# Kernel tuning notes

Hardware: AMD Instinct MI355X
Metric: run time of the kernel (lower is better)

## Reference

```python
import jax, jax.numpy as jnp
import numpy as np

B, N, D = 4, 2048, 1024
H, HD = 16, 64          # heads, head dim
ROT = 64                # rotary dims (full head)
SCALE = HD ** -0.5


def _rotate_half(x):
    # interleaved pair rotation: (c r) with r=2 -> (-x2, x1)
    x = x.reshape(x.shape[:-1] + (-1, 2))
    x1, x2 = x[..., 0], x[..., 1]
    return jnp.stack((-x2, x1), axis=-1).reshape(x.shape[:-2] + (-1,))


def _rope(t, pos_enc):
    # t: [b,h,n,c], pos_enc: [1,n,rot] -> broadcast over heads
    pe = pos_enc[:, None, : t.shape[-2], :]          # [1,1,n,rot]
    t_rot, t_pass = t[..., :ROT], t[..., ROT:]
    t_rot = t_rot * jnp.cos(pe) + _rotate_half(t_rot) * jnp.sin(pe)
    return jnp.concatenate((t_rot, t_pass), axis=-1)


def setup_inputs() -> dict:
    key = jax.random.key(0)
    ks = jax.random.split(key, 16)
    s = 0.02
    return {
        "query": jax.random.normal(ks[0], (B, N, D), jnp.float32),
        "key": jax.random.normal(ks[1], (B, N, D), jnp.float32),
        "value": jax.random.normal(ks[2], (B, N, D), jnp.float32),
        "pad_mask": jax.random.randint(ks[3], (B, N), 0, 2) > 0,
        "pos_enc": jax.random.uniform(ks[4], (1, N, ROT), jnp.float32),
        "Wq": jax.random.normal(ks[5], (D, D), jnp.float32) * s,
        "bq": jnp.zeros((D,), jnp.float32),
        "Wk": jax.random.normal(ks[6], (D, D), jnp.float32) * s,
        "bk": jnp.zeros((D,), jnp.float32),
        "Wv": jax.random.normal(ks[7], (D, D), jnp.float32) * s,
        "bv": jnp.zeros((D,), jnp.float32),
        "Wo": jax.random.normal(ks[8], (D, D), jnp.float32) * s,
        "bo": jnp.zeros((D,), jnp.float32),
    }


def reference(query, key, value, pad_mask, pos_enc, Wq, bq, Wk, bk, Wv, bv, Wo, bo):
    def split_heads(x):
        return x.reshape(x.shape[0], x.shape[1], H, HD).transpose(0, 2, 1, 3)  # b h n c

    q = split_heads(query @ Wq + bq) * SCALE
    k = split_heads(key @ Wk + bk)
    v = split_heads(value @ Wv + bv)

    q = _rope(q, pos_enc)
    k = _rope(k, pos_enc)

    attn = jnp.einsum("bhic,bhjc->bhij", q, k)
    neg = -jnp.finfo(attn.dtype).max
    attn = jnp.where(pad_mask[:, None, None, :], neg, attn)
    attn = jax.nn.softmax(attn, axis=-1)

    o = jnp.einsum("bhij,bhjc->bhic", attn, v)
    o = o.transpose(0, 2, 1, 3).reshape(o.shape[0], o.shape[2], H * HD)  # b n (h c)
    return o @ Wo + bo
```

## Files before the change

### kernel.cpp

```cpp
#include <hip/hip_runtime.h>

#define B_ 4
#define N_ 2048
#define D_ 1024
#define H_ 16
#define HD_ 64
#define QSCALE_ 0.18033688011112042f

typedef __bf16 bf16x8 __attribute__((ext_vector_type(8)));
typedef float f32x4 __attribute__((ext_vector_type(4)));

#if __has_builtin(__builtin_amdgcn_exp2f)
#define EXP2(x) __builtin_amdgcn_exp2f(x)
#else
#define EXP2(x) exp2f(x)
#endif

__device__ __forceinline__ f32x4 mfma16(bf16x8 a, bf16x8 b, f32x4 c) {
    return __builtin_amdgcn_mfma_f32_16x16x32_bf16(a, b, c, 0, 0, 0);
}

__device__ __forceinline__ void gload16(const void* g, void* l) {
    __builtin_amdgcn_global_load_lds(
        (const __attribute__((address_space(1))) void*)g,
        (__attribute__((address_space(3))) void*)l, 16, 0, 0);
}

__device__ __forceinline__ unsigned pack2(float x, float y) {
    __bf16 a = (__bf16)x, b = (__bf16)y;
    unsigned ua = __builtin_bit_cast(unsigned short, a);
    unsigned ub = __builtin_bit_cast(unsigned short, b);
    return ua | (ub << 16);
}

__global__ void prep_kernel(const float* __restrict__ pe, const int* __restrict__ mask,
                            unsigned* __restrict__ cstab, float* __restrict__ maskf) {
    int i = blockIdx.x * 256 + threadIdx.x;
    if (i < N_ * HD_) {
        float v = pe[i];
        __bf16 cb = (__bf16)cosf(v), sb = (__bf16)sinf(v);
        unsigned cu = __builtin_bit_cast(unsigned short, cb);
        unsigned su = __builtin_bit_cast(unsigned short, sb);
        cstab[i] = cu | (su << 16);
    }
    if (i < B_ * N_) maskf[i] = mask[i] ? -1e30f : 0.0f;
}

__global__ __launch_bounds__(256) void tw_kernel(const float* __restrict__ W, __bf16* __restrict__ Wt) {
    __shared__ float T[64][65];
    const int k0 = blockIdx.x * 64, n0 = blockIdx.y * 64;
    const int t = threadIdx.x;
#pragma unroll
    for (int i = 0; i < 4; ++i) {
        int row = i * 16 + (t >> 4);
        int c4 = (t & 15) * 4;
        float4 v = *(const float4*)(W + (size_t)(k0 + row) * D_ + n0 + c4);
        T[row][c4] = v.x; T[row][c4 + 1] = v.y; T[row][c4 + 2] = v.z; T[row][c4 + 3] = v.w;
    }
    __syncthreads();
#pragma unroll
    for (int i = 0; i < 2; ++i) {
        int task = i * 256 + t;
        int nrow = task >> 3, ks = task & 7;
        bf16x8 o;
#pragma unroll
        for (int e = 0; e < 8; ++e) o[e] = (__bf16)T[ks * 8 + e][nrow];
        *(bf16x8*)(Wt + (size_t)(n0 + nrow) * D_ + k0 + ks * 8) = o;
    }
}

__global__ __launch_bounds__(256) void tw3_kernel(
    const float* __restrict__ W0, const float* __restrict__ W1, const float* __restrict__ W2,
    __bf16* __restrict__ T0, __bf16* __restrict__ T1, __bf16* __restrict__ T2)
{
    const float* W = (blockIdx.z == 0) ? W0 : (blockIdx.z == 1) ? W1 : W2;
    __bf16* Wt = (blockIdx.z == 0) ? T0 : (blockIdx.z == 1) ? T1 : T2;
    __shared__ float T[64][65];
    const int k0 = blockIdx.x * 64, n0 = blockIdx.y * 64;
    const int t = threadIdx.x;
#pragma unroll
    for (int i = 0; i < 4; ++i) {
        int row = i * 16 + (t >> 4);
        int c4 = (t & 15) * 4;
        float4 v = *(const float4*)(W + (size_t)(k0 + row) * D_ + n0 + c4);
        T[row][c4] = v.x; T[row][c4 + 1] = v.y; T[row][c4 + 2] = v.z; T[row][c4 + 3] = v.w;
    }
    __syncthreads();
#pragma unroll
    for (int i = 0; i < 2; ++i) {
        int task = i * 256 + t;
        int nrow = task >> 3, ks = task & 7;
        bf16x8 o;
#pragma unroll
        for (int e = 0; e < 8; ++e) o[e] = (__bf16)T[ks * 8 + e][nrow];
        *(bf16x8*)(Wt + (size_t)(n0 + nrow) * D_ + k0 + ks * 8) = o;
    }
}

__global__ __launch_bounds__(256) void proj_v2(
    const float* __restrict__ X, const __bf16* __restrict__ Wt,
    const float* __restrict__ bias, const unsigned* __restrict__ cstab,
    __bf16* __restrict__ dst, int mode)
{
    __shared__ __align__(16) char smem[35072];
    __bf16* As = (__bf16*)smem;
    __bf16* Bs = (__bf16*)(smem + 16384);

    const int tid = threadIdx.x;
    const int lane = tid & 63, w = tid >> 6;
    const int wr = w >> 1, wc = w & 1;
    const int r16 = lane & 15, g = lane >> 4;
    const int m0 = blockIdx.x * 128;
    const int n0 = blockIdx.y * 128;
    const int srow8 = tid >> 3, slot = tid & 7;

    f32x4 acc[4][4];
#pragma unroll
    for (int m = 0; m < 4; ++m)
#pragma unroll
        for (int n = 0; n < 4; ++n) acc[m][n] = (f32x4){0.f, 0.f, 0.f, 0.f};

    for (int kt = 0; kt < 16; ++kt) {
#pragma unroll
        for (int j = 0; j < 4; ++j) {
            int row = j * 32 + srow8;
            const char* src = (const char*)Wt + ((size_t)(n0 + row) * D_ + kt * 64) * 2
                              + ((slot ^ (row & 7)) << 4);
            gload16(src, (char*)Bs + j * 4096 + w * 1024);
        }
#pragma unroll
        for (int i = 0; i < 4; ++i) {
            int row = i * 32 + srow8;
            const float* s = X + (size_t)(m0 + row) * D_ + kt * 64 + slot * 8;
            float4 v0 = *(const float4*)s;
            float4 v1 = *(const float4*)(s + 4);
            bf16x8 bv;
            bv[0] = (__bf16)v0.x; bv[1] = (__bf16)v0.y; bv[2] = (__bf16)v0.z; bv[3] = (__bf16)v0.w;
            bv[4] = (__bf16)v1.x; bv[5] = (__bf16)v1.y; bv[6] = (__bf16)v1.z; bv[7] = (__bf16)v1.w;
            *(bf16x8*)((char*)As + row * 128 + ((slot ^ (row & 7)) << 4)) = bv;
        }
        __syncthreads();
#pragma unroll
        for (int kk = 0; kk < 2; ++kk) {
            bf16x8 aF[4], bF[4];
#pragma unroll
            for (int m = 0; m < 4; ++m) {
                int row = wr * 64 + m * 16 + r16;
                aF[m] = *(const bf16x8*)((char*)As + row * 128 + (((kk * 4 + g) ^ (row & 7)) << 4));
            }
#pragma unroll
            for (int n = 0; n < 4; ++n) {
                int row = wc * 64 + n * 16 + r16;
                bF[n] = *(const bf16x8*)((char*)Bs + row * 128 + (((kk * 4 + g) ^ (row & 7)) << 4));
            }
#pragma unroll
            for (int m = 0; m < 4; ++m)
#pragma unroll
                for (int n = 0; n < 4; ++n)
                    acc[m][n] = mfma16(aF[m], bF[n], acc[m][n]);
        }
        __syncthreads();
    }

    if (mode <= 1) {
#pragma unroll
        for (int m = 0; m < 4; ++m)
#pragma unroll
            for (int n = 0; n < 4; ++n) {
                int col = n0 + wc * 64 + n * 16 + r16;
                int h = col >> 6, hd = col & 63;
#pragma unroll
                for (int j = 0; j < 4; ++j) {
                    int bn = m0 + wr * 64 + m * 16 + g * 4 + j;
                    int np = bn & (N_ - 1), b = bn >> 11;
                    float val = acc[m][n][j] + bias[col];
                    if (mode == 0) val *= QSCALE_;
                    float other = __shfl_xor(val, 1);
                    unsigned cs = cstab[np * HD_ + hd];
                    float c = __uint_as_float(cs << 16);
                    float sn = __uint_as_float(cs & 0xffff0000u);
                    val = val * c + ((col & 1) ? other : -other) * sn;
                    dst[((size_t)(b * H_ + h) * N_ + np) * HD_ + hd] = (__bf16)val;
                }
            }
    } else {
        __bf16* T = (__bf16*)smem;
#pragma unroll
        for (int m = 0; m < 4; ++m)
#pragma unroll
            for (int n = 0; n < 4; ++n) {
                int c = wc * 64 + n * 16 + r16;
                float bs = bias[n0 + c];
#pragma unroll
                for (int j = 0; j < 4; ++j) {
                    int sr = wr * 64 + m * 16 + g * 4 + j;
                    T[c * 136 + sr] = (__bf16)(acc[m][n][j] + bs);
                }
            }
        __syncthreads();
        const int b = m0 >> 11, np0 = m0 & (N_ - 1);
#pragma unroll
        for (int i = 0; i < 8; ++i) {
            int task = i * 256 + tid;
            int trow = task >> 4, ch = task & 15;
            int colg = n0 + trow;
            int h = colg >> 6, hd = colg & 63;
            bf16x8 vv = *(const bf16x8*)&T[trow * 136 + ch * 8];
            *(bf16x8*)(dst + (((size_t)(b * H_ + h) * HD_ + hd) * N_ + np0 + ch * 8)) = vv;
        }
    }
}

__global__ __launch_bounds__(256) void attn_v5(
    const __bf16* __restrict__ qws, const __bf16* __restrict__ kws,
    const __bf16* __restrict__ vtws, const float* __restrict__ maskf,
    __bf16* __restrict__ ows)
{
    __shared__ __align__(16) __bf16 Ks[2][4096];
    __shared__ __align__(16) __bf16 Vs[2][4096];
    __shared__ __align__(16) char Pbuf[8192];

    const int tid = threadIdx.x;
    const int lane = tid & 63, w = tid >> 6;
    const int r16 = lane & 15, g = lane >> 4;

    const int lid = blockIdx.x;
    const int virt = (lid & 7) * 128 + (lid >> 3);
    const int bh = virt >> 4;
    const int b = bh >> 4, h = bh & 15;
    const int q0 = (virt & 15) * 128;
    const int srow8 = tid >> 3, slot = tid & 7;

    bf16x8 qF[2][2];
#pragma unroll
    for (int qq = 0; qq < 2; ++qq) {
        const __bf16* qb = qws + ((size_t)bh * N_ + q0 + w * 32 + qq * 16 + r16) * HD_ + g * 8;
        qF[qq][0] = *(const bf16x8*)qb;
        qF[qq][1] = *(const bf16x8*)(qb + 32);
    }

    bf16x8 onesF;
#pragma unroll
    for (int e = 0; e < 8; ++e) onesF[e] = (__bf16)1.0f;

    const char* kbase = (const char*)(kws + (size_t)bh * N_ * HD_);
    const char* vbase = (const char*)(vtws + (size_t)bh * HD_ * N_);
    const float* mbase = maskf + b * N_;

    f32x4 o[2][4];
    f32x4 lacc[2];
#pragma unroll
    for (int qq = 0; qq < 2; ++qq) {
        lacc[qq] = (f32x4){0.f, 0.f, 0.f, 0.f};
#pragma unroll
        for (int n = 0; n < 4; ++n) o[qq][n] = (f32x4){0.f, 0.f, 0.f, 0.f};
    }

    auto stage = [&](int bb, int kt) {
#pragma unroll
        for (int j = 0; j < 2; ++j) {
            int row = j * 32 + srow8;
            const char* src = kbase + (size_t)(kt * 64 + row) * 128 + ((slot ^ (row & 7)) << 4);
            gload16(src, (char*)Ks[bb] + j * 4096 + w * 1024);
        }
#pragma unroll
        for (int j = 0; j < 2; ++j) {
            int row = j * 32 + srow8;
            const char* src = vbase + (size_t)row * (N_ * 2) + kt * 128 + ((slot ^ (row & 7)) << 4);
            gload16(src, (char*)Vs[bb] + j * 4096 + w * 1024);
        }
    };

    stage(0, 0);
    __syncthreads();

    int buf = 0;
    for (int kt = 0; kt < N_ / 64; ++kt) {
        if (kt + 1 < N_ / 64) stage(buf ^ 1, kt + 1);

        f32x4 s[2][4];
#pragma unroll
        for (int n = 0; n < 4; ++n) {
            s[0][n] = *(const f32x4*)(mbase + kt * 64 + n * 16 + g * 4);
            s[1][n] = *(const f32x4*)(mbase + kt * 64 + n * 16 + g * 4);
        }

        __builtin_amdgcn_s_setprio(1);
#pragma unroll
        for (int n = 0; n < 4; ++n) {
            int row = n * 16 + r16;
            bf16x8 kF0 = *(const bf16x8*)((char*)Ks[buf] + row * 128 + ((g ^ (row & 7)) << 4));
            bf16x8 kF1 = *(const bf16x8*)((char*)Ks[buf] + row * 128 + (((4 + g) ^ (row & 7)) << 4));
#pragma unroll
            for (int qq = 0; qq < 2; ++qq) {
                s[qq][n] = mfma16(kF0, qF[qq][0], s[qq][n]);
                s[qq][n] = mfma16(kF1, qF[qq][1], s[qq][n]);
            }
        }
        __builtin_amdgcn_s_setprio(0);

        bf16x8 pF[2][2];
#pragma unroll
        for (int qq = 0; qq < 2; ++qq) {
            char* Pw = Pbuf + w * 2048;
#pragma unroll
            for (int n = 0; n < 4; ++n) {
                float p0 = EXP2(s[qq][n][0]);
                float p1 = EXP2(s[qq][n][1]);
                float p2 = EXP2(s[qq][n][2]);
                float p3 = EXP2(s[qq][n][3]);
                int u0 = ((n * 2 + (g >> 1)) ^ (r16 & 7));
                int off = (g & 1) * 2;
                *(unsigned*)(Pw + r16 * 128 + u0 * 16 + off * 4)       = pack2(p0, p1);
                *(unsigned*)(Pw + r16 * 128 + u0 * 16 + (off + 1) * 4) = pack2(p2, p3);
            }
#pragma unroll
            for (int kk = 0; kk < 2; ++kk)
                pF[qq][kk] = *(const bf16x8*)(Pw + r16 * 128 + (((kk * 4 + g) ^ (r16 & 7)) << 4));
            lacc[qq] = mfma16(onesF, pF[qq][0], lacc[qq]);
            lacc[qq] = mfma16(onesF, pF[qq][1], lacc[qq]);
        }

        __builtin_amdgcn_s_setprio(1);
#pragma unroll
        for (int n = 0; n < 4; ++n) {
            int row = n * 16 + r16;
            bf16x8 vF0 = *(const bf16x8*)((char*)Vs[buf] + row * 128 + ((g ^ (row & 7)) << 4));
            bf16x8 vF1 = *(const bf16x8*)((char*)Vs[buf] + row * 128 + (((4 + g) ^ (row & 7)) << 4));
#pragma unroll
            for (int qq = 0; qq < 2; ++qq) {
                o[qq][n] = mfma16(vF0, pF[qq][0], o[qq][n]);
                o[qq][n] = mfma16(vF1, pF[qq][1], o[qq][n]);
            }
        }
        __builtin_amdgcn_s_setprio(0);
        __syncthreads();
        buf ^= 1;
    }

#pragma unroll
    for (int qq = 0; qq < 2; ++qq) {
        float inv = 1.0f / lacc[qq][0];
        char* Pw = Pbuf + w * 2048;
#pragma unroll
        for (int n = 0; n < 4; ++n) {
            int u0 = ((n * 2 + (g >> 1)) ^ (r16 & 7));
            int off = (g & 1) * 2;
            *(unsigned*)(Pw + r16 * 128 + u0 * 16 + off * 4)       = pack2(o[qq][n][0] * inv, o[qq][n][1] * inv);
            *(unsigned*)(Pw + r16 * 128 + u0 * 16 + (off + 1) * 4) = pack2(o[qq][n][2] * inv, o[qq][n][3] * inv);
        }
        int qrow = q0 + w * 32 + qq * 16 + r16;
#pragma unroll
        for (int kk = 0; kk < 2; ++kk) {
            bf16x8 v = *(const bf16x8*)(Pw + r16 * 128 + (((kk * 4 + g) ^ (r16 & 7)) << 4));
            *(bf16x8*)(ows + ((size_t)(b * N_ + qrow)) * D_ + h * HD_ + kk * 32 + g * 8) = v;
        }
    }
}

__global__ __launch_bounds__(256) void gemm_out_v2(
    const __bf16* __restrict__ A, const __bf16* __restrict__ Wt,
    const float* __restrict__ bias, float* __restrict__ out)
{
    __shared__ __align__(16) __bf16 As[8192], Bs[8192];

    const int tid = threadIdx.x;
    const int lane = tid & 63, w = tid >> 6;
    const int wr = w >> 1, wc = w & 1;
    const int r16 = lane & 15, g = lane >> 4;
    const int m0 = blockIdx.x * 128;
    const int n0 = blockIdx.y * 128;
    const int srow8 = tid >> 3, slot = tid & 7;

    f32x4 acc[4][4];
#pragma unroll
    for (int m = 0; m < 4; ++m)
#pragma unroll
        for (int n = 0; n < 4; ++n) acc[m][n] = (f32x4){0.f, 0.f, 0.f, 0.f};

    for (int kt = 0; kt < 16; ++kt) {
#pragma unroll
        for (int j = 0; j < 4; ++j) {
            int row = j * 32 + srow8;
            const char* srcA = (const char*)A + ((size_t)(m0 + row) * D_ + kt * 64) * 2
                               + ((slot ^ (row & 7)) << 4);
            gload16(srcA, (char*)As + j * 4096 + w * 1024);
            const char* srcB = (const char*)Wt + ((size_t)(n0 + row) * D_ + kt * 64) * 2
                               + ((slot ^ (row & 7)) << 4);
            gload16(srcB, (char*)Bs + j * 4096 + w * 1024);
        }
        __syncthreads();
#pragma unroll
        for (int kk = 0; kk < 2; ++kk) {
            bf16x8 aF[4], bF[4];
#pragma unroll
            for (int m = 0; m < 4; ++m) {
                int row = wr * 64 + m * 16 + r16;
                aF[m] = *(const bf16x8*)((char*)As + row * 128 + (((kk * 4 + g) ^ (row & 7)) << 4));
            }
#pragma unroll
            for (int n = 0; n < 4; ++n) {
                int row = wc * 64 + n * 16 + r16;
                bF[n] = *(const bf16x8*)((char*)Bs + row * 128 + (((kk * 4 + g) ^ (row & 7)) << 4));
            }
#pragma unroll
            for (int m = 0; m < 4; ++m)
#pragma unroll
                for (int n = 0; n < 4; ++n)
                    acc[m][n] = mfma16(aF[m], bF[n], acc[m][n]);
        }
        __syncthreads();
    }

#pragma unroll
    for (int m = 0; m < 4; ++m)
#pragma unroll
        for (int n = 0; n < 4; ++n) {
            int col = n0 + wc * 64 + n * 16 + r16;
            float bs = bias[col];
#pragma unroll
            for (int j = 0; j < 4; ++j) {
                int bn = m0 + wr * 64 + m * 16 + g * 4 + j;
                out[(size_t)bn * D_ + col] = acc[m][n][j] + bs;
            }
        }
}

extern "C" void kernel_launch(void* const* d_in, const int* in_sizes, int n_in,
                              void* d_out, int out_size, void* d_ws, size_t ws_size,
                              hipStream_t stream)
{
    const float* query = (const float*)d_in[0];
    const float* key   = (const float*)d_in[1];
    const float* value = (const float*)d_in[2];
    const int* mask    = (const int*)d_in[3];
    const float* pos_enc = (const float*)d_in[4];
    const float* Wq = (const float*)d_in[5];
    const float* bq = (const float*)d_in[6];
    const float* Wk = (const float*)d_in[7];
    const float* bk = (const float*)d_in[8];
    const float* Wv = (const float*)d_in[9];
    const float* bv = (const float*)d_in[10];
    const float* Wo = (const float*)d_in[11];
    const float* bo = (const float*)d_in[12];
    float* out = (float*)d_out;

    char* ws = (char*)d_ws;
    const size_t MB16 = (size_t)16 * 1024 * 1024;
    const size_t need = 4 * MB16 + 524288 + 32768;
    if (ws_size < need) return;

    __bf16* qws   = (__bf16*)(ws);
    __bf16* kws   = (__bf16*)(ws + MB16);
    __bf16* vtws  = (__bf16*)(ws + 2 * MB16);
    __bf16* ows   = (__bf16*)(ws + 3 * MB16);
    unsigned* cstab = (unsigned*)(ws + 4 * MB16);
    float* maskf  = (float*)(ws + 4 * MB16 + 524288);
    __bf16* wtQ   = (__bf16*)(ws + 3 * MB16);
    __bf16* wtK   = wtQ + (size_t)D_ * D_;
    __bf16* wtV   = wtK + (size_t)D_ * D_;
    __bf16* wtO   = (__bf16*)(ws);

    hipLaunchKernelGGL(prep_kernel, dim3(512), dim3(256), 0, stream, pos_enc, mask, cstab, maskf);

    dim3 gt3(16, 16, 3);
    dim3 gt(16, 16);
    dim3 gp(8192 / 128, 1024 / 128);
    hipLaunchKernelGGL(tw3_kernel, gt3, dim3(256), 0, stream, Wq, Wk, Wv, wtQ, wtK, wtV);
    hipLaunchKernelGGL(proj_v2, gp, dim3(256), 0, stream, query, wtQ, bq, cstab, qws, 0);
    hipLaunchKernelGGL(proj_v2, gp, dim3(256), 0, stream, key,   wtK, bk, cstab, kws, 1);
    hipLaunchKernelGGL(proj_v2, gp, dim3(256), 0, stream, value, wtV, bv, cstab, vtws, 2);

    hipLaunchKernelGGL(attn_v5, dim3(1024), dim3(256), 0, stream,
                       qws, kws, vtws, maskf, ows);

    hipLaunchKernelGGL(tw_kernel, gt, dim3(256), 0, stream, Wo, wtO);
    hipLaunchKernelGGL(gemm_out_v2, gp, dim3(256), 0, stream, ows, wtO, bo, out);
}
```

Baseline: 238.1 us.

## Merge Q/K/V projections into one launch and unroll attention double-buffer loop

The three separate projection launches become a single kernel whose grid's y dimension selects Q, K or V, with the weight async loads moved after the activation conversion. The attention kernel gets launch_bounds with an occupancy hint, named K/V buffers, and a manually unrolled two-tile loop so buffer indices are compile-time constants; the two query sub-tiles' softmax writes are also serialized through the shared P buffer. This is meant to cut launch overhead and tail effects and to remove dynamic LDS indexing. The occupancy hint may add register pressure.

```diff
diff --git a/kernel.cpp b/kernel.cpp
--- a/kernel.cpp
+++ b/kernel.cpp
@@ -97,21 +97,30 @@
     }
 }
 
-__global__ __launch_bounds__(256) void proj_v2(
-    const float* __restrict__ X, const __bf16* __restrict__ Wt,
-    const float* __restrict__ bias, const unsigned* __restrict__ cstab,
-    __bf16* __restrict__ dst, int mode)
+__global__ __launch_bounds__(256) void proj_v4(
+    const float* __restrict__ Xq, const float* __restrict__ Xk, const float* __restrict__ Xv,
+    const __bf16* __restrict__ WtQ, const __bf16* __restrict__ WtK, const __bf16* __restrict__ WtV,
+    const float* __restrict__ bQ, const float* __restrict__ bK, const float* __restrict__ bV,
+    const unsigned* __restrict__ cstab,
+    __bf16* __restrict__ dq, __bf16* __restrict__ dk, __bf16* __restrict__ dv)
 {
     __shared__ __align__(16) char smem[35072];
     __bf16* As = (__bf16*)smem;
     __bf16* Bs = (__bf16*)(smem + 16384);
+
+    const int which = blockIdx.y >> 3;
+    const float* X    = (which == 0) ? Xq  : (which == 1) ? Xk  : Xv;
+    const __bf16* Wt  = (which == 0) ? WtQ : (which == 1) ? WtK : WtV;
+    const float* bias = (which == 0) ? bQ  : (which == 1) ? bK  : bV;
+    __bf16* dst       = (which == 0) ? dq  : (which == 1) ? dk  : dv;
+    const int mode = which;
 
     const int tid = threadIdx.x;
     const int lane = tid & 63, w = tid >> 6;
     const int wr = w >> 1, wc = w & 1;
     const int r16 = lane & 15, g = lane >> 4;
     const int m0 = blockIdx.x * 128;
-    const int n0 = blockIdx.y * 128;
+    const int n0 = (blockIdx.y & 7) * 128;
     const int srow8 = tid >> 3, slot = tid & 7;
 
     f32x4 acc[4][4];
@@ -121,13 +130,6 @@
         for (int n = 0; n < 4; ++n) acc[m][n] = (f32x4){0.f, 0.f, 0.f, 0.f};
 
     for (int kt = 0; kt < 16; ++kt) {
-#pragma unroll
-        for (int j = 0; j < 4; ++j) {
-            int row = j * 32 + srow8;
-            const char* src = (const char*)Wt + ((size_t)(n0 + row) * D_ + kt * 64) * 2
-                              + ((slot ^ (row & 7)) << 4);
-            gload16(src, (char*)Bs + j * 4096 + w * 1024);
-        }
 #pragma unroll
         for (int i = 0; i < 4; ++i) {
             int row = i * 32 + srow8;
@@ -138,6 +140,13 @@
             bv[0] = (__bf16)v0.x; bv[1] = (__bf16)v0.y; bv[2] = (__bf16)v0.z; bv[3] = (__bf16)v0.w;
             bv[4] = (__bf16)v1.x; bv[5] = (__bf16)v1.y; bv[6] = (__bf16)v1.z; bv[7] = (__bf16)v1.w;
             *(bf16x8*)((char*)As + row * 128 + ((slot ^ (row & 7)) << 4)) = bv;
+        }
+#pragma unroll
+        for (int j = 0; j < 4; ++j) {
+            int row = j * 32 + srow8;
+            const char* src = (const char*)Wt + ((size_t)(n0 + row) * D_ + kt * 64) * 2
+                              + ((slot ^ (row & 7)) << 4);
+            gload16(src, (char*)Bs + j * 4096 + w * 1024);
         }
         __syncthreads();
 #pragma unroll
@@ -211,13 +220,13 @@
     }
 }
 
-__global__ __launch_bounds__(256) void attn_v5(
+__global__ __launch_bounds__(256, 4) void attn_v6(
     const __bf16* __restrict__ qws, const __bf16* __restrict__ kws,
     const __bf16* __restrict__ vtws, const float* __restrict__ maskf,
     __bf16* __restrict__ ows)
 {
-    __shared__ __align__(16) __bf16 Ks[2][4096];
-    __shared__ __align__(16) __bf16 Vs[2][4096];
+    __shared__ __align__(16) __bf16 Ks0[4096], Ks1[4096];
+    __shared__ __align__(16) __bf16 Vs0[4096], Vs1[4096];
     __shared__ __align__(16) char Pbuf[8192];
 
     const int tid = threadIdx.x;
@@ -246,6 +255,7 @@
     const char* kbase = (const char*)(kws + (size_t)bh * N_ * HD_);
     const char* vbase = (const char*)(vtws + (size_t)bh * HD_ * N_);
     const float* mbase = maskf + b * N_;
+    char* Pw = Pbuf + w * 2048;
 
     f32x4 o[2][4];
     f32x4 lacc[2];
@@ -256,92 +266,92 @@
         for (int n = 0; n < 4; ++n) o[qq][n] = (f32x4){0.f, 0.f, 0.f, 0.f};
     }
 
-    auto stage = [&](int bb, int kt) {
-#pragma unroll
-        for (int j = 0; j < 2; ++j) {
-            int row = j * 32 + srow8;
-            const char* src = kbase + (size_t)(kt * 64 + row) * 128 + ((slot ^ (row & 7)) << 4);
-            gload16(src, (char*)Ks[bb] + j * 4096 + w * 1024);
-        }
-#pragma unroll
-        for (int j = 0; j < 2; ++j) {
-            int row = j * 32 + srow8;
-            const char* src = vbase + (size_t)row * (N_ * 2) + kt * 128 + ((slot ^ (row & 7)) << 4);
-            gload16(src, (char*)Vs[bb] + j * 4096 + w * 1024);
-        }
-    };
-
-    stage(0, 0);
+#define STAGE_(KD, VD, kt) {                                                          \
+    _Pragma("unroll")                                                                 \
+    for (int j = 0; j < 2; ++j) {                                                     \
+        int row = j * 32 + srow8;                                                     \
+        gload16(kbase + (size_t)((kt) * 64 + row) * 128 + ((slot ^ (row & 7)) << 4),  \
+                (char*)(KD) + j * 4096 + w * 1024);                                   \
+    }                                                                                 \
+    _Pragma("unroll")                                                                 \
+    for (int j = 0; j < 2; ++j) {                                                     \
+        int row = j * 32 + srow8;                                                     \
+        gload16(vbase + (size_t)row * (N_ * 2) + (kt) * 128 + ((slot ^ (row & 7)) << 4), \
+                (char*)(VD) + j * 4096 + w * 1024);                                   \
+    } }
+
+#define TILE_(KB, VB, KN, VN, kt) {                                                   \
+    if ((kt) + 1 < 32) STAGE_(KN, VN, (kt) + 1);                                      \
+    f32x4 s0[4], s1[4];                                                               \
+    _Pragma("unroll")                                                                 \
+    for (int n = 0; n < 4; ++n) {                                                     \
+        f32x4 mb = *(const f32x4*)(mbase + (kt) * 64 + n * 16 + g * 4);               \
+        s0[n] = mb; s1[n] = mb;                                                       \
+    }                                                                                 \
+    __builtin_amdgcn_s_setprio(1);                                                    \
+    _Pragma("unroll")                                                                 \
+    for (int n = 0; n < 4; ++n) {                                                     \
+        int row = n * 16 + r16;                                                       \
+        bf16x8 kF0 = *(const bf16x8*)((const char*)(KB) + row * 128 + ((g ^ (row & 7)) << 4));        \
+        bf16x8 kF1 = *(const bf16x8*)((const char*)(KB) + row * 128 + (((4 + g) ^ (row & 7)) << 4));  \
+        s0[n] = mfma16(kF0, qF[0][0], s0[n]);                                         \
+        s0[n] = mfma16(kF1, qF[0][1], s0[n]);                                         \
+        s1[n] = mfma16(kF0, qF[1][0], s1[n]);                                         \
+        s1[n] = mfma16(kF1, qF[1][1], s1[n]);                                         \
+    }                                                                                 \
+    __builtin_amdgcn_s_setprio(0);                                                    \
+    bf16x8 pF0[2], pF1[2];                                                            \
+    _Pragma("unroll")                                                                 \
+    for (int n = 0; n < 4; ++n) {                                                     \
+        int u0 = ((n * 2 + (g >> 1)) ^ (r16 & 7));                                    \
+        int off = (g & 1) * 2;                                                        \
+        *(unsigned*)(Pw + r16 * 128 + u0 * 16 + off * 4)       = pack2(EXP2(s0[n][0]), EXP2(s0[n][1])); \
+        *(unsigned*)(Pw + r16 * 128 + u0 * 16 + (off + 1) * 4) = pack2(EXP2(s0[n][2]), EXP2(s0[n][3])); \
+    }                                                                                 \
+    _Pragma("unroll")                                                                 \
+    for (int kk = 0; kk < 2; ++kk)                                                    \
+        pF0[kk] = *(const bf16x8*)(Pw + r16 * 128 + (((kk * 4 + g) ^ (r16 & 7)) << 4)); \
+    lacc[0] = mfma16(onesF, pF0[0], lacc[0]);                                         \
+    lacc[0] = mfma16(onesF, pF0[1], lacc[0]);                                         \
+    _Pragma("unroll")                                                                 \
+    for (int n = 0; n < 4; ++n) {                                                     \
+        int u0 = ((n * 2 + (g >> 1)) ^ (r16 & 7));                                    \
+        int off = (g & 1) * 2;                                                        \
+        *(unsigned*)(Pw + r16 * 128 + u0 * 16 + off * 4)       = pack2(EXP2(s1[n][0]), EXP2(s1[n][1])); \
+        *(unsigned*)(Pw + r16 * 128 + u0 * 16 + (off + 1) * 4) = pack2(EXP2(s1[n][2]), EXP2(s1[n][3])); \
+    }                                                                                 \
+    _Pragma("unroll")                                                                 \
+    for (int kk = 0; kk < 2; ++kk)                                                    \
+        pF1[kk] = *(const bf16x8*)(Pw + r16 * 128 + (((kk * 4 + g) ^ (r16 & 7)) << 4)); \
+    lacc[1] = mfma16(onesF, pF1[0], lacc[1]);                                         \
+    lacc[1] = mfma16(onesF, pF1[1], lacc[1]);                                         \
+    __builtin_amdgcn_s_setprio(1);                                                    \
+    _Pragma("unroll")                                                                 \
+    for (int n = 0; n < 4; ++n) {                                                     \
+        int row = n * 16 + r16;                                                       \
+        bf16x8 vF0 = *(const bf16x8*)((const char*)(VB) + row * 128 + ((g ^ (row & 7)) << 4));        \
+        bf16x8 vF1 = *(const bf16x8*)((const char*)(VB) + row * 128 + (((4 + g) ^ (row & 7)) << 4));  \
+        o[0][n] = mfma16(vF0, pF0[0], o[0][n]);                                       \
+        o[0][n] = mfma16(vF1, pF0[1], o[0][n]);                                       \
+        o[1][n] = mfma16(vF0, pF1[0], o[1][n]);                                       \
+        o[1][n] = mfma16(vF1, pF1[1], o[1][n]);                                       \
+    }                                                                                 \
+    __builtin_amdgcn_s_setprio(0);                                                    \
+    __syncthreads(); }
+
+    STAGE_(Ks0, Vs0, 0);
     __syncthreads();
 
-    int buf = 0;
-    for (int kt = 0; kt < N_ / 64; ++kt) {
-        if (kt + 1 < N_ / 64) stage(buf ^ 1, kt + 1);
-
-        f32x4 s[2][4];
-#pragma unroll
-        for (int n = 0; n < 4; ++n) {
-            s[0][n] = *(const f32x4*)(mbase + kt * 64 + n * 16 + g * 4);
-            s[1][n] = *(const f32x4*)(mbase + kt * 64 + n * 16 + g * 4);
-        }
-
-        __builtin_amdgcn_s_setprio(1);
-#pragma unroll
-        for (int n = 0; n < 4; ++n) {
-            int row = n * 16 + r16;
-            bf16x8 kF0 = *(const bf16x8*)((char*)Ks[buf] + row * 128 + ((g ^ (row & 7)) << 4));
-            bf16x8 kF1 = *(const bf16x8*)((char*)Ks[buf] + row * 128 + (((4 + g) ^ (row & 7)) << 4));
-#pragma unroll
-            for (int qq = 0; qq < 2; ++qq) {
-                s[qq][n] = mfma16(kF0, qF[qq][0], s[qq][n]);
-                s[qq][n] = mfma16(kF1, qF[qq][1], s[qq][n]);
-            }
-        }
-        __builtin_amdgcn_s_setprio(0);
-
-        bf16x8 pF[2][2];
-#pragma unroll
-        for (int qq = 0; qq < 2; ++qq) {
-            char* Pw = Pbuf + w * 2048;
-#pragma unroll
-            for (int n = 0; n < 4; ++n) {
-                float p0 = EXP2(s[qq][n][0]);
-                float p1 = EXP2(s[qq][n][1]);
-                float p2 = EXP2(s[qq][n][2]);
-                float p3 = EXP2(s[qq][n][3]);
-                int u0 = ((n * 2 + (g >> 1)) ^ (r16 & 7));
-                int off = (g & 1) * 2;
-                *(unsigned*)(Pw + r16 * 128 + u0 * 16 + off * 4)       = pack2(p0, p1);
-                *(unsigned*)(Pw + r16 * 128 + u0 * 16 + (off + 1) * 4) = pack2(p2, p3);
-            }
-#pragma unroll
-            for (int kk = 0; kk < 2; ++kk)
-                pF[qq][kk] = *(const bf16x8*)(Pw + r16 * 128 + (((kk * 4 + g) ^ (r16 & 7)) << 4));
-            lacc[qq] = mfma16(onesF, pF[qq][0], lacc[qq]);
-            lacc[qq] = mfma16(onesF, pF[qq][1], lacc[qq]);
-        }
-
-        __builtin_amdgcn_s_setprio(1);
-#pragma unroll
-        for (int n = 0; n < 4; ++n) {
-            int row = n * 16 + r16;
-            bf16x8 vF0 = *(const bf16x8*)((char*)Vs[buf] + row * 128 + ((g ^ (row & 7)) << 4));
-            bf16x8 vF1 = *(const bf16x8*)((char*)Vs[buf] + row * 128 + (((4 + g) ^ (row & 7)) << 4));
-#pragma unroll
-            for (int qq = 0; qq < 2; ++qq) {
-                o[qq][n] = mfma16(vF0, pF[qq][0], o[qq][n]);
-                o[qq][n] = mfma16(vF1, pF[qq][1], o[qq][n]);
-            }
-        }
-        __builtin_amdgcn_s_setprio(0);
-        __syncthreads();
-        buf ^= 1;
-    }
+    for (int kt = 0; kt < 32; kt += 2) {
+        TILE_(Ks0, Vs0, Ks1, Vs1, kt);
+        TILE_(Ks1, Vs1, Ks0, Vs0, kt + 1);
+    }
+#undef TILE_
+#undef STAGE_
 
 #pragma unroll
     for (int qq = 0; qq < 2; ++qq) {
         float inv = 1.0f / lacc[qq][0];
-        char* Pw = Pbuf + w * 2048;
 #pragma unroll
         for (int n = 0; n < 4; ++n) {
             int u0 = ((n * 2 + (g >> 1)) ^ (r16 & 7));
@@ -465,15 +475,14 @@
 
     dim3 gt3(16, 16, 3);
     dim3 gt(16, 16);
-    dim3 gp(8192 / 128, 1024 / 128);
     hipLaunchKernelGGL(tw3_kernel, gt3, dim3(256), 0, stream, Wq, Wk, Wv, wtQ, wtK, wtV);
-    hipLaunchKernelGGL(proj_v2, gp, dim3(256), 0, stream, query, wtQ, bq, cstab, qws, 0);
-    hipLaunchKernelGGL(proj_v2, gp, dim3(256), 0, stream, key,   wtK, bk, cstab, kws, 1);
-    hipLaunchKernelGGL(proj_v2, gp, dim3(256), 0, stream, value, wtV, bv, cstab, vtws, 2);
-
-    hipLaunchKernelGGL(attn_v5, dim3(1024), dim3(256), 0, stream,
+
+    hipLaunchKernelGGL(proj_v4, dim3(64, 24), dim3(256), 0, stream,
+                       query, key, value, wtQ, wtK, wtV, bq, bk, bv, cstab, qws, kws, vtws);
+
+    hipLaunchKernelGGL(attn_v6, dim3(1024), dim3(256), 0, stream,
                        qws, kws, vtws, maskf, ows);
 
     hipLaunchKernelGGL(tw_kernel, gt, dim3(256), 0, stream, Wo, wtO);
-    hipLaunchKernelGGL(gemm_out_v2, gp, dim3(256), 0, stream, ows, wtO, bo, out);
-}
+    hipLaunchKernelGGL(gemm_out_v2, dim3(64, 8), dim3(256), 0, stream, ows, wtO, bo, out);
+}
```

After: 222.7 us. 1.07x faster.
